# Performance work log

Measured on AMD Instinct MI355X. Metric: run time of the kernel, lower is better.

Reference implementation:

```python
import jax, jax.numpy as jnp
import numpy as np

B, S = 2, 2048
D_MODEL = 1024
N_HEADS = 16
N_VALUES = 8192
D_RETR = 128
MAX_POS = 2048


def setup_inputs() -> dict:
    key = jax.random.key(0)
    ks = jax.random.split(key, 10)
    s = 0.02
    return {
        "hidden_states": jax.random.normal(ks[0], (B, S, D_MODEL), jnp.float32),
        "attention_mask": jnp.ones((B, S), jnp.float32),
        "Wq": jax.random.normal(ks[1], (D_MODEL, D_MODEL), jnp.float32) * s,
        "bq": jnp.zeros((D_MODEL,), jnp.float32),
        "Wk": jax.random.normal(ks[2], (D_MODEL, D_MODEL), jnp.float32) * s,
        "bk": jnp.zeros((D_MODEL,), jnp.float32),
        # torch init is round(ones)=all ones; use random 0/1 so the per-head dynamic mask is exercised
        "dynamic_mask": jnp.round(jax.random.uniform(ks[3], (N_HEADS, MAX_POS), jnp.float32)),
        "Wvq": jax.random.normal(ks[4], (D_MODEL, D_RETR), jnp.float32) * s,
        "bvq": jnp.zeros((D_RETR,), jnp.float32),
        "v_keys": jax.random.normal(ks[5], (N_VALUES, D_RETR), jnp.float32) * s,
        "v_embed": jax.random.normal(ks[6], (N_VALUES, D_MODEL), jnp.float32) * s,
        "Wo": jax.random.normal(ks[7], (D_MODEL, D_MODEL), jnp.float32) * s,
        "bo": jnp.zeros((D_MODEL,), jnp.float32),
    }


def reference(hidden_states, attention_mask, Wq, bq, Wk, bk, dynamic_mask,
              Wvq, bvq, v_keys, v_embed, Wo, bo):
    b, s, d = hidden_states.shape
    h = dynamic_mask.shape[0]
    hd = d // h
    dtype = hidden_states.dtype
    min_d = jnp.finfo(dtype).min

    q = (hidden_states @ Wq + bq).reshape(b, s, h, hd).transpose(0, 2, 1, 3)  # [B,H,S,hd]
    k = (hidden_states @ Wk + bk).reshape(b, s, h, hd).transpose(0, 2, 1, 3)

    # inner_func: top-1 codebook value retrieval
    vq = hidden_states @ Wvq + bvq                      # [B,S,Dr]
    sim = jnp.einsum('bsr,nr->bsn', vq, v_keys)         # [B,S,Nv]
    idx = jnp.argmax(sim, axis=-1)                      # top-1 indices [B,S]
    v = hidden_states * v_embed[idx]                    # [B,S,D]
    v = v.reshape(b, s, h, hd).transpose(0, 2, 1, 3)    # [B,H,S,hd]

    # 4D causal mask fused with per-head dynamic mask and padding mask
    tgt = attention_mask.shape[-1]
    causal = jnp.where(jnp.arange(tgt)[None, :] > jnp.arange(s)[:, None],
                       min_d, jnp.array(0, dtype))[None, None]        # [1,1,S,S]
    am = attention_mask[:, None, None, :] * dynamic_mask[None, :, None, :tgt]  # [B,H,1,S]
    padding = causal + am                                              # [B,H,S,S]
    mask = jnp.where(padding == 0, min_d, causal)                      # [B,H,S,S]

    scores = jnp.einsum('bhqd,bhkd->bhqk', q, k) / jnp.sqrt(jnp.array(hd, dtype))
    scores = scores + mask
    w = jax.nn.softmax(scores.astype(jnp.float32), axis=-1).astype(dtype)

    out = jnp.einsum('bhqk,bhkd->bhqd', w, v)            # [B,H,S,hd]
    out = out.transpose(0, 2, 1, 3).reshape(b, s, d)
    return out @ Wo + bo
```

## Files before the change

### kernel.cpp

```cpp
#include <hip/hip_runtime.h>
#include <hip/hip_bf16.h>
#include <math.h>

#define MIN_D (-3.402823466e+38f)

constexpr int Bb = 2, Ss = 2048, Dm = 1024, Hh = 16, HDd = 64, NV = 8192, DRr = 128;
constexpr int Mrows = Bb * Ss;
constexpr float MARGIN = 0.01f;
constexpr int CAP = 65536;
constexpr float C2 = 0.18033688011112042f;

typedef __attribute__((ext_vector_type(8))) short bf16x8;
typedef __attribute__((ext_vector_type(4))) float f32x4;

__device__ inline unsigned short f2bf(float x) {
    union { float f; unsigned u; } v; v.f = x;
    unsigned r = v.u + 0x7fff + ((v.u >> 16) & 1);
    return (unsigned short)(r >> 16);
}
__device__ inline float bf2f(unsigned short u) {
    union { unsigned u; float f; } v; v.u = ((unsigned)u) << 16;
    return v.f;
}
__device__ inline unsigned pk_bf16(float a, float b) {
    float2 t; t.x = a; t.y = b;
    __hip_bfloat162 h = __float22bfloat162_rn(t);
    return *(unsigned*)&h;
}

__global__ __launch_bounds__(256)
void cvt_bf16(const float* __restrict__ x, unsigned short* __restrict__ y)
{
    size_t i = ((size_t)blockIdx.x * 256 + threadIdx.x) * 8;
    float4 a = *(const float4*)(x + i);
    float4 b = *(const float4*)(x + i + 4);
    uint4 p;
    p.x = pk_bf16(a.x, a.y);
    p.y = pk_bf16(a.z, a.w);
    p.z = pk_bf16(b.x, b.y);
    p.w = pk_bf16(b.z, b.w);
    *(uint4*)(y + i) = p;
}

__global__ __launch_bounds__(256)
void transpose_cvt3(const float* __restrict__ W0, const float* __restrict__ W1,
                    const float* __restrict__ W2, unsigned short* __restrict__ T0,
                    unsigned short* __restrict__ T1, unsigned short* __restrict__ T2)
{
    const float* W = blockIdx.z == 0 ? W0 : (blockIdx.z == 1 ? W1 : W2);
    unsigned short* WT = blockIdx.z == 0 ? T0 : (blockIdx.z == 1 ? T1 : T2);
    __shared__ unsigned short T[64][72];
    const int tid = threadIdx.x;
    const int n0 = blockIdx.x * 64, k0 = blockIdx.y * 64;
    const int rr = tid >> 4, cc = tid & 15;
#pragma unroll
    for (int q2 = 0; q2 < 4; ++q2) {
        int kk = rr * 4 + q2;
        float4 v = *(const float4*)(W + (size_t)(k0 + kk) * Dm + n0 + cc * 4);
        T[cc * 4 + 0][kk] = f2bf(v.x);
        T[cc * 4 + 1][kk] = f2bf(v.y);
        T[cc * 4 + 2][kk] = f2bf(v.z);
        T[cc * 4 + 3][kk] = f2bf(v.w);
    }
    __syncthreads();
#pragma unroll
    for (int q2 = 0; q2 < 4; ++q2) {
        int nn = rr * 4 + q2;
        uint2 u;
        u.x = (unsigned)T[nn][cc * 4 + 0] | ((unsigned)T[nn][cc * 4 + 1] << 16);
        u.y = (unsigned)T[nn][cc * 4 + 2] | ((unsigned)T[nn][cc * 4 + 3] << 16);
        *(uint2*)(WT + (size_t)(n0 + nn) * Dm + k0 + cc * 4) = u;
    }
}

template<bool BF16OUT>
__global__ __launch_bounds__(512)
void gemm_bf16(const unsigned short* __restrict__ A,
               const unsigned short* BT0, const unsigned short* BT1,
               const float* bias0, const float* bias1,
               void* C0, void* C1, int N, int K)
{
    const unsigned short* BT = blockIdx.z ? BT1 : BT0;
    const float* bias = blockIdx.z ? bias1 : bias0;
    void* C = blockIdx.z ? C1 : C0;
    __shared__ __align__(16) unsigned short As[128 * 32];
    __shared__ __align__(16) unsigned short Bs[128 * 32];
    const int tid = threadIdx.x;
    const int l = tid & 63, w = tid >> 6;
    const int l15 = l & 15, l4 = l >> 4;
    const int wm = w >> 2, wn = w & 3;
    const int row0 = blockIdx.y * 128, col0 = blockIdx.x * 128;

    f32x4 acc[4][2];
#pragma unroll
    for (int mi = 0; mi < 4; ++mi)
#pragma unroll
        for (int ni = 0; ni < 2; ++ni) acc[mi][ni] = (f32x4)(0.f);

    for (int k0 = 0; k0 < K; k0 += 32) {
        __syncthreads();
        {
            int r = tid >> 2, pc = tid & 3;
            uint4 vv = *(const uint4*)(A + (size_t)(row0 + r) * K + k0 + pc * 8);
            *(uint4*)&As[tid * 8] = vv;
        }
        {
            int r = tid >> 2, pc = tid & 3;
            uint4 vv = *(const uint4*)(BT + (size_t)(col0 + r) * K + k0 + pc * 8);
            *(uint4*)&Bs[tid * 8] = vv;
        }
        __syncthreads();

        bf16x8 af[4], bf[2];
#pragma unroll
        for (int mi = 0; mi < 4; ++mi)
            af[mi] = *(bf16x8*)&As[(wm * 64 + mi * 16 + l15) * 32 + l4 * 8];
#pragma unroll
        for (int ni = 0; ni < 2; ++ni)
            bf[ni] = *(bf16x8*)&Bs[(wn * 32 + ni * 16 + l15) * 32 + l4 * 8];
#pragma unroll
        for (int mi = 0; mi < 4; ++mi)
#pragma unroll
            for (int ni = 0; ni < 2; ++ni)
                acc[mi][ni] = __builtin_amdgcn_mfma_f32_16x16x32_bf16(af[mi], bf[ni], acc[mi][ni], 0, 0, 0);
    }

#pragma unroll
    for (int mi = 0; mi < 4; ++mi)
#pragma unroll
        for (int ni = 0; ni < 2; ++ni)
#pragma unroll
            for (int j = 0; j < 4; ++j) {
                int row = row0 + wm * 64 + mi * 16 + l4 * 4 + j;
                int col = col0 + wn * 32 + ni * 16 + l15;
                float vv = acc[mi][ni][j] + bias[col];
                if (BF16OUT)
                    ((unsigned short*)C)[(size_t)row * N + col] = f2bf(vv);
                else
                    ((float*)C)[(size_t)row * N + col] = vv;
            }
}

__global__ __launch_bounds__(256)
void gemm_vq_partial(const float* __restrict__ A, const float* __restrict__ W,
                     float* __restrict__ P)
{
    __shared__ float As[64][36];
    __shared__ float Ws[32][64];
    const int tid = threadIdx.x;
    const int row0 = blockIdx.y * 64, col0 = blockIdx.x * 64;
    const int kbase = blockIdx.z * 256;
    const int tr = tid >> 4, tc = tid & 15;
    float acc[4][4] = {};

    for (int k0 = kbase; k0 < kbase + 256; k0 += 32) {
        __syncthreads();
#pragma unroll
        for (int q2 = 0; q2 < 2; ++q2) {
            int oc = q2 * 256 + tid;
            int r = oc >> 3, c4 = (oc & 7) << 2;
            *(float4*)&As[r][c4] = *(const float4*)(A + (size_t)(row0 + r) * Dm + k0 + c4);
        }
#pragma unroll
        for (int q2 = 0; q2 < 2; ++q2) {
            int oc = q2 * 256 + tid;
            int r = oc >> 4, c4 = (oc & 15) << 2;
            *(float4*)&Ws[r][c4] = *(const float4*)(W + (size_t)(k0 + r) * DRr + col0 + c4);
        }
        __syncthreads();
#pragma unroll 8
        for (int kk = 0; kk < 32; ++kk) {
            float a[4];
#pragma unroll
            for (int i = 0; i < 4; ++i) a[i] = As[tr * 4 + i][kk];
            float4 bv = *(const float4*)&Ws[kk][tc * 4];
            float b[4] = {bv.x, bv.y, bv.z, bv.w};
#pragma unroll
            for (int i = 0; i < 4; ++i)
#pragma unroll
                for (int j = 0; j < 4; ++j)
                    acc[i][j] = fmaf(a[i], b[j], acc[i][j]);
        }
    }
    float* Pz = P + (size_t)blockIdx.z * Mrows * DRr;
#pragma unroll
    for (int i = 0; i < 4; ++i) {
        int r = row0 + tr * 4 + i;
        float4 ov = {acc[i][0], acc[i][1], acc[i][2], acc[i][3]};
        *(float4*)(Pz + (size_t)r * DRr + col0 + tc * 4) = ov;
    }
}

__global__ __launch_bounds__(256)
void reduce_vq(const float* __restrict__ P, const float* __restrict__ bias,
               float* __restrict__ vqb, unsigned short* __restrict__ vq_hi)
{
    const size_t i4 = ((size_t)blockIdx.x * 256 + threadIdx.x) * 4;
    const int col = (int)(i4 & 127);
    const size_t stride = (size_t)Mrows * DRr;
    float4 s = *(const float4*)(P + i4);
#pragma unroll
    for (int z = 1; z < 4; ++z) {
        float4 p = *(const float4*)(P + stride * z + i4);
        s.x += p.x; s.y += p.y; s.z += p.z; s.w += p.w;
    }
    float4 bv = *(const float4*)(bias + col);
    s.x += bv.x; s.y += bv.y; s.z += bv.z; s.w += bv.w;
    *(float4*)(vqb + i4) = s;
    uint2 u;
    u.x = pk_bf16(s.x, s.y);
    u.y = pk_bf16(s.z, s.w);
    *(uint2*)(vq_hi + i4) = u;
}

template<int PASS>
__global__ __launch_bounds__(256)
void sim_pass(const unsigned short* __restrict__ vq_hi,
              const unsigned short* __restrict__ vk_hi,
              float* __restrict__ pm1,
              unsigned* __restrict__ cnt, unsigned* __restrict__ pairs)
{
    __shared__ __align__(16) unsigned short VQs[64 * 128];
    __shared__ __align__(16) unsigned short Ks[64 * 128];
    __shared__ float thrs[64];
    const int tid = threadIdx.x;
    const int l = tid & 63, w = tid >> 6;
    const int l15 = l & 15, l4 = l >> 4;
    const int row0 = blockIdx.x * 64;
    const int key0 = blockIdx.y * 1024;
    const int qloc = w * 16 + l15;
    const int q = row0 + qloc;

    if (PASS == 1 && tid < 64) {
        const float* pp = pm1 + (size_t)(row0 + tid) * 8;
        float m = pp[0];
#pragma unroll
        for (int c = 1; c < 8; ++c) m = fmaxf(m, pp[c]);
        thrs[tid] = m - MARGIN;
    }
#pragma unroll
    for (int q2 = 0; q2 < 4; ++q2) {
        int oc = q2 * 256 + tid;
        int r = oc >> 4, pc = oc & 15;
        int lc = pc ^ (r & 7);
        uint4 vv = *(const uint4*)(vq_hi + (size_t)(row0 + r) * 128 + lc * 8);
        *(uint4*)&VQs[oc * 8] = vv;
    }
    __syncthreads();
    bf16x8 qf[4];
#pragma unroll
    for (int kk = 0; kk < 4; ++kk)
        qf[kk] = *(bf16x8*)&VQs[qloc * 128 + (((kk * 4 + l4) ^ (qloc & 7)) * 8)];

    float th = (PASS == 1) ? thrs[qloc] : 0.f;
    float vmax = -INFINITY;

    for (int t = 0; t < 16; ++t) {
        __syncthreads();
#pragma unroll
        for (int q2 = 0; q2 < 4; ++q2) {
            int oc = q2 * 256 + tid;
            int r = oc >> 4, pc = oc & 15;
            int lc = pc ^ (r & 7);
            uint4 vv = *(const uint4*)(vk_hi + (size_t)(key0 + t * 64 + r) * 128 + lc * 8);
            *(uint4*)&Ks[oc * 8] = vv;
        }
        __syncthreads();
#pragma unroll
        for (int kb = 0; kb < 4; ++kb) {
            const int key16 = kb * 16 + l15;
            f32x4 s = (f32x4)(0.f);
#pragma unroll
            for (int kk = 0; kk < 4; ++kk) {
                bf16x8 kfr = *(bf16x8*)&Ks[key16 * 128 + (((kk * 4 + l4) ^ (key16 & 7)) * 8)];
                s = __builtin_amdgcn_mfma_f32_16x16x32_bf16(kfr, qf[kk], s, 0, 0, 0);
            }
            if (PASS == 0) {
#pragma unroll
                for (int r = 0; r < 4; ++r) vmax = fmaxf(vmax, s[r]);
            } else {
#pragma unroll
                for (int r = 0; r < 4; ++r) {
                    if (s[r] >= th) {
                        int key = key0 + t * 64 + kb * 16 + l4 * 4 + r;
                        unsigned slot = atomicAdd(cnt, 1u);
                        if (slot < (unsigned)CAP)
                            pairs[slot] = ((unsigned)q << 13) | (unsigned)key;
                    }
                }
            }
        }
    }
    if (PASS == 0) {
        vmax = fmaxf(vmax, __shfl_xor(vmax, 16));
        vmax = fmaxf(vmax, __shfl_xor(vmax, 32));
        if (l4 == 0) pm1[(size_t)q * 8 + blockIdx.y] = vmax;
    }
}

__global__ __launch_bounds__(256)
void sim_rescore(const unsigned* __restrict__ pairs, const unsigned* __restrict__ cnt,
                 const float* __restrict__ vq, const float* __restrict__ vkeys,
                 unsigned long long* __restrict__ best)
{
    const int l = threadIdx.x & 63;
    const unsigned wav = (blockIdx.x * 256 + threadIdx.x) >> 6;
    const unsigned nw = (gridDim.x * 256) >> 6;
    const unsigned n = min(*cnt, (unsigned)CAP);
    for (unsigned i = wav; i < n; i += nw) {
        unsigned p = pairs[i];
        unsigned row = p >> 13, key = p & 8191u;
        float2 a = *(const float2*)(vq + (size_t)row * 128 + l * 2);
        float2 b = *(const float2*)(vkeys + (size_t)key * 128 + l * 2);
        float d = a.x * b.x + a.y * b.y;
#pragma unroll
        for (int off = 32; off; off >>= 1) d += __shfl_xor(d, off);
        if (l == 0) {
            unsigned fb = __float_as_uint(d);
            fb = (fb & 0x80000000u) ? ~fb : (fb | 0x80000000u);
            unsigned long long enc = ((unsigned long long)fb << 32) | (unsigned)(~key);
            atomicMax(best + row, enc);
        }
    }
}

__global__ __launch_bounds__(256)
void build_vt(const float* __restrict__ hs, const float* __restrict__ vembed,
              const unsigned long long* __restrict__ best,
              unsigned short* __restrict__ vt)
{
    __shared__ unsigned short T[64][73];
    __shared__ int ids[64];
    const int tid = threadIdx.x;
    const int kt = blockIdx.x;
    const int bh = blockIdx.y;
    const int b = bh >> 4, h = bh & 15;
    if (tid < 64) {
        int row = b * Ss + kt * 64 + tid;
        ids[tid] = (int)((~(unsigned)(best[row] & 0xFFFFFFFFull)) & 8191u);
    }
    __syncthreads();
    {
        int r = tid >> 2, c16 = (tid & 3) * 16;
        size_t hrow = (size_t)(b * Ss + kt * 64 + r) * Dm + h * HDd + c16;
        size_t erow = (size_t)ids[r] * Dm + h * HDd + c16;
#pragma unroll
        for (int q2 = 0; q2 < 4; ++q2) {
            float4 a = *(const float4*)(hs + hrow + q2 * 4);
            float4 e = *(const float4*)(vembed + erow + q2 * 4);
            T[r][c16 + q2 * 4 + 0] = f2bf(a.x * e.x);
            T[r][c16 + q2 * 4 + 1] = f2bf(a.y * e.y);
            T[r][c16 + q2 * 4 + 2] = f2bf(a.z * e.z);
            T[r][c16 + q2 * 4 + 3] = f2bf(a.w * e.w);
        }
    }
    __syncthreads();
    {
        int d = tid >> 2, kc = (tid & 3) * 16;
        unsigned short ob[16];
#pragma unroll
        for (int i = 0; i < 16; ++i) ob[i] = T[kc + i][d];
        unsigned short* op = vt + ((size_t)(b * Hh + h) * HDd + d) * Ss + kt * 64 + kc;
        *(uint4*)op = *(uint4*)&ob[0];
        *(uint4*)(op + 8) = *(uint4*)&ob[8];
    }
}

__global__ __launch_bounds__(256)
void mean_vt(const unsigned short* __restrict__ vt, float* __restrict__ mv)
{
    const int bh = blockIdx.x;
    const int b = bh >> 4, h = bh & 15;
    const int d = threadIdx.x >> 2, part = threadIdx.x & 3;
    const unsigned short* row = vt + ((size_t)bh * HDd + d) * Ss + part * 512;
    float s = 0.f;
    for (int j = 0; j < 512; j += 8) {
        uint4 u = *(const uint4*)(row + j);
        const unsigned uu[4] = {u.x, u.y, u.z, u.w};
#pragma unroll
        for (int m = 0; m < 4; ++m) {
            s += bf2f((unsigned short)(uu[m] & 0xffff));
            s += bf2f((unsigned short)(uu[m] >> 16));
        }
    }
    s += __shfl_xor(s, 1);
    s += __shfl_xor(s, 2);
    if (part == 0) mv[b * Dm + h * HDd + d] = s * (1.f / 2048.f);
}

__global__ __launch_bounds__(512)
void attn_mfma4(const unsigned short* __restrict__ q, const unsigned short* __restrict__ k,
                const unsigned short* __restrict__ vt, const float* __restrict__ am,
                const float* __restrict__ dmask, const float* __restrict__ meanv,
                unsigned short* __restrict__ o)
{
    __shared__ __align__(16) unsigned char smem[40960];
    __shared__ float uniflag[128];
    unsigned char* Ksm = smem;
    unsigned char* Vsm = smem + 8192;
    unsigned char* Psm = smem + 16384;
    float* amdmf = (float*)(smem + 32768);

    const int tid = threadIdx.x;
    const int l = tid & 63, w = tid >> 6;
    const int l15 = l & 15, l4 = l >> 4;
    const int lin = blockIdx.x + (blockIdx.y << 4) + (blockIdx.z << 8);
    const int half = lin >> 8, rem = lin & 255;
    const int qtb = rem & 15;
    const int qt = half ? (15 - qtb) : qtb;
    const int h = rem >> 4;
    const int b = half;
    const int row0 = qt * 128;

    {
        int j = tid * 4;
        float4 a = *(const float4*)(am + b * Ss + j);
        float4 d = *(const float4*)(dmask + h * Ss + j);
        float4 m;
        m.x = (a.x * d.x == 0.f) ? MIN_D : 0.f;
        m.y = (a.y * d.y == 0.f) ? MIN_D : 0.f;
        m.z = (a.z * d.z == 0.f) ? MIN_D : 0.f;
        m.w = (a.w * d.w == 0.f) ? MIN_D : 0.f;
        *(float4*)&amdmf[j] = m;
    }

    const int qloc = w * 16 + l15;
    const int qrow = row0 + qloc;
    bf16x8 qf[2];
    {
        const unsigned short* qp = q + ((size_t)(b * Ss + qrow)) * Dm + h * HDd + l4 * 8;
        qf[0] = *(const bf16x8*)qp;
        qf[1] = *(const bf16x8*)(qp + 32);
    }

    f32x4 acc[4];
#pragma unroll
    for (int d2 = 0; d2 < 4; ++d2) acc[d2] = (f32x4)(0.f);
    float mrun = -INFINITY, lrun = 0.f;
    const int ktmax = 2 * qt + 1;

    for (int kt = 0; kt <= ktmax; ++kt) {
        __syncthreads();
        {
            int key = tid >> 3, pc = tid & 7, lc = pc ^ (key & 7);
            uint4 vv = *(const uint4*)(k + ((size_t)(b * Ss + kt * 64 + key)) * Dm
                                       + h * HDd + lc * 8);
            *(uint4*)&Ksm[tid * 16] = vv;
        }
        {
            int d = tid >> 3, pc = tid & 7, lc = pc ^ (d & 7);
            uint4 vv = *(const uint4*)(vt + ((size_t)(b * Hh + h) * HDd + d) * Ss
                                       + kt * 64 + lc * 8);
            *(uint4*)&Vsm[tid * 16] = vv;
        }
        __syncthreads();

        f32x4 sreg[4];
#pragma unroll
        for (int kb = 0; kb < 4; ++kb) {
            const int key16 = kb * 16 + l15;
            const int sw = key16 & 7;
            bf16x8 k0 = *(bf16x8*)&Ksm[key16 * 128 + ((l4 ^ sw) * 16)];
            bf16x8 k1 = *(bf16x8*)&Ksm[key16 * 128 + (((4 + l4) ^ sw) * 16)];
            f32x4 s = (f32x4)(0.f);
            s = __builtin_amdgcn_mfma_f32_16x16x32_bf16(k0, qf[0], s, 0, 0, 0);
            s = __builtin_amdgcn_mfma_f32_16x16x32_bf16(k1, qf[1], s, 0, 0, 0);
            sreg[kb] = s;
        }

        float sv[16];
#pragma unroll
        for (int kb = 0; kb < 4; ++kb)
#pragma unroll
            for (int r = 0; r < 4; ++r) {
                const int key = kt * 64 + kb * 16 + l4 * 4 + r;
                const float mval = (key > qrow) ? MIN_D : amdmf[key];
                sv[kb * 4 + r] = fmaf(sreg[kb][r], C2, mval);
            }

        float pm = fmaxf(fmaxf(sv[0], sv[1]), sv[2]);
        pm = fmaxf(fmaxf(pm, sv[3]), fmaxf(sv[4], sv[5]));
        pm = fmaxf(fmaxf(pm, sv[6]), fmaxf(sv[7], sv[8]));
        pm = fmaxf(fmaxf(pm, sv[9]), fmaxf(sv[10], sv[11]));
        pm = fmaxf(fmaxf(pm, sv[12]), fmaxf(sv[13], sv[14]));
        pm = fmaxf(pm, sv[15]);
        pm = fmaxf(pm, __shfl_xor(pm, 16));
        pm = fmaxf(pm, __shfl_xor(pm, 32));

        if (__any(pm > mrun + 8.f)) {
            const float mn = fmaxf(mrun, pm);
            const float sc = __builtin_amdgcn_exp2f(mrun - mn);
            lrun *= sc;
#pragma unroll
            for (int d2 = 0; d2 < 4; ++d2) acc[d2] *= sc;
            mrun = mn;
        }

        float p[16], rs = 0.f;
#pragma unroll
        for (int i = 0; i < 16; ++i) {
            p[i] = __builtin_amdgcn_exp2f(sv[i] - mrun);
            rs += p[i];
        }
        rs += __shfl_xor(rs, 16);
        rs += __shfl_xor(rs, 32);
        lrun += rs;

        const unsigned pswz = (l15 & 7) << 4;
#pragma unroll
        for (int kb = 0; kb < 4; ++kb) {
            uint2 u;
            u.x = pk_bf16(p[kb * 4 + 0], p[kb * 4 + 1]);
            u.y = pk_bf16(p[kb * 4 + 2], p[kb * 4 + 3]);
            *(uint2*)&Psm[qloc * 128 + ((kb * 32 + l4 * 8) ^ pswz)] = u;
        }

#pragma unroll
        for (int ks = 0; ks < 2; ++ks) {
            bf16x8 pa = *(bf16x8*)&Psm[qloc * 128 + ((ks * 64 + l4 * 16) ^ pswz)];
#pragma unroll
            for (int d2 = 0; d2 < 4; ++d2) {
                const int dd = d2 * 16 + l15;
                bf16x8 vb = *(bf16x8*)&Vsm[dd * 128 + ((ks * 64 + l4 * 16) ^ ((dd & 7) << 4))];
                acc[d2] = __builtin_amdgcn_mfma_f32_16x16x32_bf16(vb, pa, acc[d2], 0, 0, 0);
            }
        }
    }

    const float inv = 1.f / lrun;
    const bool uni = (mrun <= -1e37f);
    __syncthreads();
    unsigned short* stg = (unsigned short*)smem;
    uniflag[qloc] = uni ? 1.f : 0.f;
#pragma unroll
    for (int d2 = 0; d2 < 4; ++d2) {
        uint2 u;
        u.x = pk_bf16(acc[d2][0] * inv, acc[d2][1] * inv);
        u.y = pk_bf16(acc[d2][2] * inv, acc[d2][3] * inv);
        *(uint2*)&stg[qloc * 72 + d2 * 16 + l4 * 4] = u;
    }
    __syncthreads();
    {
        const int r = tid >> 2, c16 = (tid & 3) * 16;
        const bool u = uniflag[r] != 0.f;
        uint4 o0, o1;
        if (u) {
            unsigned short ob[16];
#pragma unroll
            for (int i = 0; i < 16; ++i)
                ob[i] = f2bf(meanv[b * Dm + h * HDd + c16 + i]);
            o0 = *(uint4*)&ob[0];
            o1 = *(uint4*)&ob[8];
        } else {
            o0 = *(uint4*)&stg[r * 72 + c16];
            o1 = *(uint4*)&stg[r * 72 + c16 + 8];
        }
        unsigned short* op = o + ((size_t)(b * Ss + row0 + r)) * Dm + h * HDd + c16;
        *(uint4*)op = o0;
        *(uint4*)(op + 8) = o1;
    }
}

extern "C" void kernel_launch(void* const* d_in, const int* in_sizes, int n_in,
                              void* d_out, int out_size, void* d_ws, size_t ws_size,
                              hipStream_t stream)
{
    const float* hs     = (const float*)d_in[0];
    const float* amask  = (const float*)d_in[1];
    const float* Wq     = (const float*)d_in[2];
    const float* bq     = (const float*)d_in[3];
    const float* Wk     = (const float*)d_in[4];
    const float* bk     = (const float*)d_in[5];
    const float* dmask  = (const float*)d_in[6];
    const float* Wvq    = (const float*)d_in[7];
    const float* bvq    = (const float*)d_in[8];
    const float* vkeys  = (const float*)d_in[9];
    const float* vembed = (const float*)d_in[10];
    const float* Wo     = (const float*)d_in[11];
    const float* bo     = (const float*)d_in[12];
    float* out = (float*)d_out;

    char* w = (char*)d_ws;
    size_t off = 0;
    auto take = [&](size_t n) { char* p = w + off; off = (off + n + 255) & ~(size_t)255; return p; };
    unsigned short* hsbf  = (unsigned short*)take((size_t)Mrows * Dm * 2);
    unsigned short* WqT   = (unsigned short*)take((size_t)Dm * Dm * 2);
    unsigned short* WkT   = (unsigned short*)take((size_t)Dm * Dm * 2);
    unsigned short* WoT   = (unsigned short*)take((size_t)Dm * Dm * 2);
    unsigned short* qbf   = (unsigned short*)take((size_t)Mrows * Dm * 2);
    unsigned short* kbf   = (unsigned short*)take((size_t)Mrows * Dm * 2);
    unsigned short* vtb   = (unsigned short*)take((size_t)Mrows * Dm * 2);
    unsigned short* attno = (unsigned short*)take((size_t)Mrows * Dm * 2);
    float* vqp   = (float*)take((size_t)4 * Mrows * DRr * 4);
    float* vqb   = (float*)take((size_t)Mrows * DRr * 4);
    unsigned short* vq_hi = (unsigned short*)take((size_t)Mrows * DRr * 2);
    unsigned short* vk_hi = (unsigned short*)take((size_t)NV * DRr * 2);
    float* pm1   = (float*)take((size_t)Mrows * 8 * 4);
    unsigned* cnt = (unsigned*)take(256);
    unsigned* pairs = (unsigned*)take((size_t)CAP * 4);
    unsigned long long* best = (unsigned long long*)take((size_t)Mrows * 8);
    float* mvb   = (float*)take((size_t)Bb * Dm * 4);

    hipMemsetAsync(cnt, 0, 4, stream);
    hipMemsetAsync(best, 0, (size_t)Mrows * 8, stream);

    dim3 blk(256);
    cvt_bf16<<<dim3(Mrows * Dm / 2048), blk, 0, stream>>>(hs, hsbf);
    transpose_cvt3<<<dim3(Dm / 64, Dm / 64, 3), blk, 0, stream>>>(Wq, Wk, Wo, WqT, WkT, WoT);
    gemm_bf16<true><<<dim3(Dm / 128, Mrows / 128, 2), dim3(512), 0, stream>>>(
        hsbf, WqT, WkT, bq, bk, qbf, kbf, Dm, Dm);
    gemm_vq_partial<<<dim3(DRr / 64, Mrows / 64, 4), blk, 0, stream>>>(hs, Wvq, vqp);
    reduce_vq<<<dim3(Mrows * DRr / 1024), blk, 0, stream>>>(vqp, bvq, vqb, vq_hi);
    cvt_bf16<<<dim3(NV * DRr / 2048), blk, 0, stream>>>(vkeys, vk_hi);
    sim_pass<0><<<dim3(Mrows / 64, 8), blk, 0, stream>>>(vq_hi, vk_hi, pm1, nullptr, nullptr);
    sim_pass<1><<<dim3(Mrows / 64, 8), blk, 0, stream>>>(vq_hi, vk_hi, pm1, cnt, pairs);
    sim_rescore<<<dim3(256), blk, 0, stream>>>(pairs, cnt, vqb, vkeys, best);
    build_vt<<<dim3(Ss / 64, Bb * Hh), blk, 0, stream>>>(hs, vembed, best, vtb);
    mean_vt<<<dim3(Bb * Hh), blk, 0, stream>>>(vtb, mvb);
    attn_mfma4<<<dim3(Ss / 128, Hh, Bb), dim3(512), 0, stream>>>(
        qbf, kbf, vtb, amask, dmask, mvb, attno);
    gemm_bf16<false><<<dim3(Dm / 128, Mrows / 128, 1), dim3(512), 0, stream>>>(
        attno, WoT, WoT, bo, bo, out, out, Dm, Dm);
}
```

Before: 267.2 us.

## Double-buffer key tiles in sim passes and split key range across more blocks

The two codebook-similarity passes now prefetch the next 64-key tile into registers while MFMAs run on the current tile. The tile is then written to the other half of a shared double buffer, so each iteration needs one barrier instead of two. The key dimension is also split 16 ways instead of 8, which doubles the grid and halves each block's loop, and the per-row partial-max buffer is widened to match. This is meant to hide global-load latency and raise occupancy and parallelism. The cost is extra register pressure for the staged tile and twice as many partial maxima to reduce in pass 1.

```diff
diff --git a/kernel.cpp b/kernel.cpp
--- a/kernel.cpp
+++ b/kernel.cpp
@@ -220,22 +220,21 @@
               float* __restrict__ pm1,
               unsigned* __restrict__ cnt, unsigned* __restrict__ pairs)
 {
-    __shared__ __align__(16) unsigned short VQs[64 * 128];
-    __shared__ __align__(16) unsigned short Ks[64 * 128];
+    __shared__ __align__(16) unsigned short Buf[2][64 * 128];
     __shared__ float thrs[64];
     const int tid = threadIdx.x;
     const int l = tid & 63, w = tid >> 6;
     const int l15 = l & 15, l4 = l >> 4;
     const int row0 = blockIdx.x * 64;
-    const int key0 = blockIdx.y * 1024;
+    const int key0 = blockIdx.y * 512;
     const int qloc = w * 16 + l15;
     const int q = row0 + qloc;
 
     if (PASS == 1 && tid < 64) {
-        const float* pp = pm1 + (size_t)(row0 + tid) * 8;
+        const float* pp = pm1 + (size_t)(row0 + tid) * 16;
         float m = pp[0];
 #pragma unroll
-        for (int c = 1; c < 8; ++c) m = fmaxf(m, pp[c]);
+        for (int c = 1; c < 16; ++c) m = fmaxf(m, pp[c]);
         thrs[tid] = m - MARGIN;
     }
 #pragma unroll
@@ -244,35 +243,52 @@
         int r = oc >> 4, pc = oc & 15;
         int lc = pc ^ (r & 7);
         uint4 vv = *(const uint4*)(vq_hi + (size_t)(row0 + r) * 128 + lc * 8);
-        *(uint4*)&VQs[oc * 8] = vv;
+        *(uint4*)&Buf[0][oc * 8] = vv;
     }
     __syncthreads();
     bf16x8 qf[4];
 #pragma unroll
     for (int kk = 0; kk < 4; ++kk)
-        qf[kk] = *(bf16x8*)&VQs[qloc * 128 + (((kk * 4 + l4) ^ (qloc & 7)) * 8)];
+        qf[kk] = *(bf16x8*)&Buf[0][qloc * 128 + (((kk * 4 + l4) ^ (qloc & 7)) * 8)];
+    {
+        const int r = tid >> 2, pc4 = tid & 3;
+#pragma unroll
+        for (int q2 = 0; q2 < 4; ++q2) {
+            int rr = (q2 << 4) + r;
+        }
+    }
+#pragma unroll
+    for (int q2 = 0; q2 < 4; ++q2) {
+        int oc = q2 * 256 + tid;
+        int r = oc >> 4, pc = oc & 15;
+        int lc = pc ^ (r & 7);
+        uint4 vv = *(const uint4*)(vk_hi + (size_t)(key0 + r) * 128 + lc * 8);
+        *(uint4*)&Buf[1][oc * 8] = vv;
+    }
+    __syncthreads();
 
     float th = (PASS == 1) ? thrs[qloc] : 0.f;
     float vmax = -INFINITY;
 
-    for (int t = 0; t < 16; ++t) {
-        __syncthreads();
-#pragma unroll
-        for (int q2 = 0; q2 < 4; ++q2) {
-            int oc = q2 * 256 + tid;
-            int r = oc >> 4, pc = oc & 15;
-            int lc = pc ^ (r & 7);
-            uint4 vv = *(const uint4*)(vk_hi + (size_t)(key0 + t * 64 + r) * 128 + lc * 8);
-            *(uint4*)&Ks[oc * 8] = vv;
-        }
-        __syncthreads();
+    for (int t = 0; t < 8; ++t) {
+        const int cur = (t & 1) ^ 1;
+        uint4 st[4];
+        if (t + 1 < 8) {
+#pragma unroll
+            for (int q2 = 0; q2 < 4; ++q2) {
+                int oc = q2 * 256 + tid;
+                int r = oc >> 4, pc = oc & 15;
+                int lc = pc ^ (r & 7);
+                st[q2] = *(const uint4*)(vk_hi + (size_t)(key0 + (t + 1) * 64 + r) * 128 + lc * 8);
+            }
+        }
 #pragma unroll
         for (int kb = 0; kb < 4; ++kb) {
             const int key16 = kb * 16 + l15;
             f32x4 s = (f32x4)(0.f);
 #pragma unroll
             for (int kk = 0; kk < 4; ++kk) {
-                bf16x8 kfr = *(bf16x8*)&Ks[key16 * 128 + (((kk * 4 + l4) ^ (key16 & 7)) * 8)];
+                bf16x8 kfr = *(bf16x8*)&Buf[cur][key16 * 128 + (((kk * 4 + l4) ^ (key16 & 7)) * 8)];
                 s = __builtin_amdgcn_mfma_f32_16x16x32_bf16(kfr, qf[kk], s, 0, 0, 0);
             }
             if (PASS == 0) {
@@ -290,11 +306,19 @@
                 }
             }
         }
+        if (t + 1 < 8) {
+#pragma unroll
+            for (int q2 = 0; q2 < 4; ++q2) {
+                int oc = q2 * 256 + tid;
+                *(uint4*)&Buf[cur ^ 1][oc * 8] = st[q2];
+            }
+        }
+        __syncthreads();
     }
     if (PASS == 0) {
         vmax = fmaxf(vmax, __shfl_xor(vmax, 16));
         vmax = fmaxf(vmax, __shfl_xor(vmax, 32));
-        if (l4 == 0) pm1[(size_t)q * 8 + blockIdx.y] = vmax;
+        if (l4 == 0) pm1[(size_t)q * 16 + blockIdx.y] = vmax;
     }
 }
 
@@ -595,7 +619,7 @@
     float* vqb   = (float*)take((size_t)Mrows * DRr * 4);
     unsigned short* vq_hi = (unsigned short*)take((size_t)Mrows * DRr * 2);
     unsigned short* vk_hi = (unsigned short*)take((size_t)NV * DRr * 2);
-    float* pm1   = (float*)take((size_t)Mrows * 8 * 4);
+    float* pm1   = (float*)take((size_t)Mrows * 16 * 4);
     unsigned* cnt = (unsigned*)take(256);
     unsigned* pairs = (unsigned*)take((size_t)CAP * 4);
     unsigned long long* best = (unsigned long long*)take((size_t)Mrows * 8);
@@ -612,8 +636,8 @@
     gemm_vq_partial<<<dim3(DRr / 64, Mrows / 64, 4), blk, 0, stream>>>(hs, Wvq, vqp);
     reduce_vq<<<dim3(Mrows * DRr / 1024), blk, 0, stream>>>(vqp, bvq, vqb, vq_hi);
     cvt_bf16<<<dim3(NV * DRr / 2048), blk, 0, stream>>>(vkeys, vk_hi);
-    sim_pass<0><<<dim3(Mrows / 64, 8), blk, 0, stream>>>(vq_hi, vk_hi, pm1, nullptr, nullptr);
-    sim_pass<1><<<dim3(Mrows / 64, 8), blk, 0, stream>>>(vq_hi, vk_hi, pm1, cnt, pairs);
+    sim_pass<0><<<dim3(Mrows / 64, 16), blk, 0, stream>>>(vq_hi, vk_hi, pm1, nullptr, nullptr);
+    sim_pass<1><<<dim3(Mrows / 64, 16), blk, 0, stream>>>(vq_hi, vk_hi, pm1, cnt, pairs);
     sim_rescore<<<dim3(256), blk, 0, stream>>>(pairs, cnt, vqb, vkeys, best);
     build_vt<<<dim3(Ss / 64, Bb * Hh), blk, 0, stream>>>(hs, vembed, best, vtb);
     mean_vt<<<dim3(Bb * Hh), blk, 0, stream>>>(vtb, mvb);
```

After: 266.9 us. Within noise of the previous version (-0.1%).

## Retile codebook similarity passes as 128x128 MFMA GEMM tiles with separate threshold combine

Applied to the files above, without the earlier changes.

Replaces the 64-query by 1024-key streaming similarity kernels with a conventional 128x128 tiled MFMA GEMM over the 8192 codebook keys, using 512 threads and a K-loop of 32. Pass 0 writes a per-row max for each column tile, a new small kernel reduces those maxima into per-row thresholds, and pass 1 recomputes the tiles and appends candidate pairs above the threshold. The intent is better register-level reuse and more blocks in flight for the similarity GEMM. In exchange it adds a kernel launch and a larger row-tile-max buffer, and raises the candidate-pair capacity.

```diff
diff --git a/kernel.cpp b/kernel.cpp
--- a/kernel.cpp
+++ b/kernel.cpp
@@ -7,7 +7,7 @@
 constexpr int Bb = 2, Ss = 2048, Dm = 1024, Hh = 16, HDd = 64, NV = 8192, DRr = 128;
 constexpr int Mrows = Bb * Ss;
 constexpr float MARGIN = 0.01f;
-constexpr int CAP = 65536;
+constexpr int CAP = 262144;
 constexpr float C2 = 0.18033688011112042f;
 
 typedef __attribute__((ext_vector_type(8))) short bf16x8;
@@ -214,88 +214,117 @@
 }
 
 template<int PASS>
-__global__ __launch_bounds__(256)
-void sim_pass(const unsigned short* __restrict__ vq_hi,
-              const unsigned short* __restrict__ vk_hi,
-              float* __restrict__ pm1,
+__global__ __launch_bounds__(512)
+void sim_gemm(const unsigned short* __restrict__ A,
+              const unsigned short* __restrict__ BT,
+              float* __restrict__ rowtilemax, const float* __restrict__ thr,
               unsigned* __restrict__ cnt, unsigned* __restrict__ pairs)
 {
-    __shared__ __align__(16) unsigned short VQs[64 * 128];
-    __shared__ __align__(16) unsigned short Ks[64 * 128];
-    __shared__ float thrs[64];
+    __shared__ __align__(16) unsigned short As[128 * 32];
+    __shared__ __align__(16) unsigned short Bs[128 * 32];
+    __shared__ float red[128][4];
+    __shared__ float thrsm[128];
     const int tid = threadIdx.x;
     const int l = tid & 63, w = tid >> 6;
     const int l15 = l & 15, l4 = l >> 4;
-    const int row0 = blockIdx.x * 64;
-    const int key0 = blockIdx.y * 1024;
-    const int qloc = w * 16 + l15;
-    const int q = row0 + qloc;
-
-    if (PASS == 1 && tid < 64) {
-        const float* pp = pm1 + (size_t)(row0 + tid) * 8;
-        float m = pp[0];
-#pragma unroll
-        for (int c = 1; c < 8; ++c) m = fmaxf(m, pp[c]);
-        thrs[tid] = m - MARGIN;
-    }
-#pragma unroll
-    for (int q2 = 0; q2 < 4; ++q2) {
-        int oc = q2 * 256 + tid;
-        int r = oc >> 4, pc = oc & 15;
-        int lc = pc ^ (r & 7);
-        uint4 vv = *(const uint4*)(vq_hi + (size_t)(row0 + r) * 128 + lc * 8);
-        *(uint4*)&VQs[oc * 8] = vv;
-    }
-    __syncthreads();
-    bf16x8 qf[4];
-#pragma unroll
-    for (int kk = 0; kk < 4; ++kk)
-        qf[kk] = *(bf16x8*)&VQs[qloc * 128 + (((kk * 4 + l4) ^ (qloc & 7)) * 8)];
-
-    float th = (PASS == 1) ? thrs[qloc] : 0.f;
-    float vmax = -INFINITY;
-
-    for (int t = 0; t < 16; ++t) {
-        __syncthreads();
-#pragma unroll
-        for (int q2 = 0; q2 < 4; ++q2) {
-            int oc = q2 * 256 + tid;
-            int r = oc >> 4, pc = oc & 15;
-            int lc = pc ^ (r & 7);
-            uint4 vv = *(const uint4*)(vk_hi + (size_t)(key0 + t * 64 + r) * 128 + lc * 8);
-            *(uint4*)&Ks[oc * 8] = vv;
-        }
-        __syncthreads();
-#pragma unroll
-        for (int kb = 0; kb < 4; ++kb) {
-            const int key16 = kb * 16 + l15;
-            f32x4 s = (f32x4)(0.f);
-#pragma unroll
-            for (int kk = 0; kk < 4; ++kk) {
-                bf16x8 kfr = *(bf16x8*)&Ks[key16 * 128 + (((kk * 4 + l4) ^ (key16 & 7)) * 8)];
-                s = __builtin_amdgcn_mfma_f32_16x16x32_bf16(kfr, qf[kk], s, 0, 0, 0);
-            }
-            if (PASS == 0) {
-#pragma unroll
-                for (int r = 0; r < 4; ++r) vmax = fmaxf(vmax, s[r]);
-            } else {
-#pragma unroll
-                for (int r = 0; r < 4; ++r) {
-                    if (s[r] >= th) {
-                        int key = key0 + t * 64 + kb * 16 + l4 * 4 + r;
+    const int wm = w >> 2, wn = w & 3;
+    const int row0 = blockIdx.y * 128, col0 = blockIdx.x * 128;
+
+    if (PASS == 1 && tid < 128) thrsm[tid] = thr[row0 + tid];
+
+    f32x4 acc[4][2];
+#pragma unroll
+    for (int mi = 0; mi < 4; ++mi)
+#pragma unroll
+        for (int ni = 0; ni < 2; ++ni) acc[mi][ni] = (f32x4)(0.f);
+
+    for (int k0 = 0; k0 < DRr; k0 += 32) {
+        __syncthreads();
+        {
+            int r = tid >> 2, pc = tid & 3;
+            uint4 vv = *(const uint4*)(A + (size_t)(row0 + r) * DRr + k0 + pc * 8);
+            *(uint4*)&As[tid * 8] = vv;
+        }
+        {
+            int r = tid >> 2, pc = tid & 3;
+            uint4 vv = *(const uint4*)(BT + (size_t)(col0 + r) * DRr + k0 + pc * 8);
+            *(uint4*)&Bs[tid * 8] = vv;
+        }
+        __syncthreads();
+
+        bf16x8 af[4], bf[2];
+#pragma unroll
+        for (int mi = 0; mi < 4; ++mi)
+            af[mi] = *(bf16x8*)&As[(wm * 64 + mi * 16 + l15) * 32 + l4 * 8];
+#pragma unroll
+        for (int ni = 0; ni < 2; ++ni)
+            bf[ni] = *(bf16x8*)&Bs[(wn * 32 + ni * 16 + l15) * 32 + l4 * 8];
+#pragma unroll
+        for (int mi = 0; mi < 4; ++mi)
+#pragma unroll
+            for (int ni = 0; ni < 2; ++ni)
+                acc[mi][ni] = __builtin_amdgcn_mfma_f32_16x16x32_bf16(af[mi], bf[ni], acc[mi][ni], 0, 0, 0);
+    }
+
+    if (PASS == 0) {
+        float rm[4][4];
+#pragma unroll
+        for (int mi = 0; mi < 4; ++mi)
+#pragma unroll
+            for (int j = 0; j < 4; ++j)
+                rm[mi][j] = fmaxf(acc[mi][0][j], acc[mi][1][j]);
+#pragma unroll
+        for (int off = 1; off < 16; off <<= 1)
+#pragma unroll
+            for (int mi = 0; mi < 4; ++mi)
+#pragma unroll
+                for (int j = 0; j < 4; ++j)
+                    rm[mi][j] = fmaxf(rm[mi][j], __shfl_xor(rm[mi][j], off));
+        if (l15 == 0) {
+#pragma unroll
+            for (int mi = 0; mi < 4; ++mi)
+#pragma unroll
+                for (int j = 0; j < 4; ++j)
+                    red[wm * 64 + mi * 16 + l4 * 4 + j][wn] = rm[mi][j];
+        }
+        __syncthreads();
+        if (tid < 128) {
+            float m = fmaxf(fmaxf(red[tid][0], red[tid][1]),
+                            fmaxf(red[tid][2], red[tid][3]));
+            rowtilemax[(size_t)(row0 + tid) * 64 + blockIdx.x] = m;
+        }
+    } else {
+        __syncthreads();
+#pragma unroll
+        for (int mi = 0; mi < 4; ++mi)
+#pragma unroll
+            for (int ni = 0; ni < 2; ++ni)
+#pragma unroll
+                for (int j = 0; j < 4; ++j) {
+                    const int rl = wm * 64 + mi * 16 + l4 * 4 + j;
+                    if (acc[mi][ni][j] >= thrsm[rl]) {
+                        const int col = col0 + wn * 32 + ni * 16 + l15;
                         unsigned slot = atomicAdd(cnt, 1u);
                         if (slot < (unsigned)CAP)
-                            pairs[slot] = ((unsigned)q << 13) | (unsigned)key;
+                            pairs[slot] = ((unsigned)(row0 + rl) << 13) | (unsigned)col;
                     }
                 }
-            }
-        }
-    }
-    if (PASS == 0) {
-        vmax = fmaxf(vmax, __shfl_xor(vmax, 16));
-        vmax = fmaxf(vmax, __shfl_xor(vmax, 32));
-        if (l4 == 0) pm1[(size_t)q * 8 + blockIdx.y] = vmax;
-    }
+    }
+}
+
+__global__ __launch_bounds__(256)
+void sim_combine2(const float* __restrict__ rtm, float* __restrict__ thr)
+{
+    int r = blockIdx.x * 256 + threadIdx.x;
+    if (r >= Mrows) return;
+    const float4* p = (const float4*)(rtm + (size_t)r * 64);
+    float m = -INFINITY;
+#pragma unroll
+    for (int c = 0; c < 16; ++c) {
+        float4 v = p[c];
+        m = fmaxf(m, fmaxf(fmaxf(v.x, v.y), fmaxf(v.z, v.w)));
+    }
+    thr[r] = m - MARGIN;
 }
 
 __global__ __launch_bounds__(256)
@@ -595,7 +624,8 @@
     float* vqb   = (float*)take((size_t)Mrows * DRr * 4);
     unsigned short* vq_hi = (unsigned short*)take((size_t)Mrows * DRr * 2);
     unsigned short* vk_hi = (unsigned short*)take((size_t)NV * DRr * 2);
-    float* pm1   = (float*)take((size_t)Mrows * 8 * 4);
+    float* rtm   = (float*)take((size_t)Mrows * 64 * 4);
+    float* thr   = (float*)take((size_t)Mrows * 4);
     unsigned* cnt = (unsigned*)take(256);
     unsigned* pairs = (unsigned*)take((size_t)CAP * 4);
     unsigned long long* best = (unsigned long long*)take((size_t)Mrows * 8);
@@ -612,8 +642,11 @@
     gemm_vq_partial<<<dim3(DRr / 64, Mrows / 64, 4), blk, 0, stream>>>(hs, Wvq, vqp);
     reduce_vq<<<dim3(Mrows * DRr / 1024), blk, 0, stream>>>(vqp, bvq, vqb, vq_hi);
     cvt_bf16<<<dim3(NV * DRr / 2048), blk, 0, stream>>>(vkeys, vk_hi);
-    sim_pass<0><<<dim3(Mrows / 64, 8), blk, 0, stream>>>(vq_hi, vk_hi, pm1, nullptr, nullptr);
-    sim_pass<1><<<dim3(Mrows / 64, 8), blk, 0, stream>>>(vq_hi, vk_hi, pm1, cnt, pairs);
+    sim_gemm<0><<<dim3(NV / 128, Mrows / 128), dim3(512), 0, stream>>>(
+        vq_hi, vk_hi, rtm, nullptr, nullptr, nullptr);
+    sim_combine2<<<dim3(Mrows / 256), blk, 0, stream>>>(rtm, thr);
+    sim_gemm<1><<<dim3(NV / 128, Mrows / 128), dim3(512), 0, stream>>>(
+        vq_hi, vk_hi, nullptr, thr, cnt, pairs);
     sim_rescore<<<dim3(256), blk, 0, stream>>>(pairs, cnt, vqb, vkeys, best);
     build_vt<<<dim3(Ss / 64, Bb * Hh), blk, 0, stream>>>(hs, vembed, best, vtb);
     mean_vt<<<dim3(Bb * Hh), blk, 0, stream>>>(vtb, mvb);
```

New measurement: 277.4 us. 1.04x slower.
